# Performance work log

Hardware: AMD Instinct MI355X
Metric: run time of the kernel (lower is better)

Reference implementation:

```python
import jax, jax.numpy as jnp
import numpy as np


def setup_inputs() -> dict:
    key = jax.random.key(0)
    k1, k2, k3, k4, k5 = jax.random.split(key, 5)
    B, C, H, W = 8, 256, 64, 64
    Cp = C // 8  # query/key channels
    x = jax.random.normal(k1, (B, C, H, W), dtype=jnp.float32)
    # 1x1 conv weights (bias=False in the module), spectral norm treated as a fixed weight scale
    Wq = jax.random.normal(k2, (Cp, C), dtype=jnp.float32) * 0.05
    Wk = jax.random.normal(k3, (Cp, C), dtype=jnp.float32) * 0.05
    Wv = jax.random.normal(k4, (C, C), dtype=jnp.float32) * 0.05
    gamma = jax.random.normal(k5, (1,), dtype=jnp.float32)
    return {"x": x, "Wq": Wq, "Wk": Wk, "Wv": Wv, "gamma": gamma}


def reference(x, Wq, Wk, Wv, gamma):
    B, C, H, W = x.shape
    xf = x.reshape(B, C, H * W)  # (B, C, N)
    # ConvLayer = 1x1 conv (no bias) followed by ReLU
    f = jax.nn.relu(jnp.einsum('oc,bcn->bon', Wq, xf))  # (B, C', N)
    g = jax.nn.relu(jnp.einsum('oc,bcn->bon', Wk, xf))  # (B, C', N)
    h = jax.nn.relu(jnp.einsum('oc,bcn->bon', Wv, xf))  # (B, C, N)
    # beta = softmax(f^T g, dim=1): normalize over the FIRST N axis (faithful to source)
    scores = jnp.einsum('bcn,bcm->bnm', f, g)  # (B, N, N)
    beta = jax.nn.softmax(scores, axis=1)
    o = gamma * jnp.einsum('bcn,bnm->bcm', h, beta) + xf  # (B, C, N)
    return o.reshape(B, C, H, W)
```

## Files before the change

### kernel.cpp

```cpp
#include <hip/hip_runtime.h>


typedef __attribute__((ext_vector_type(8))) short bf16x8;
typedef __attribute__((ext_vector_type(4))) float f32x4;
typedef __attribute__((ext_vector_type(4))) unsigned short us4;

#define LOG2E 1.44269504088896f

static __device__ __forceinline__ unsigned short f2bf(float x) {
    union { float f; unsigned u; } v; v.f = x;
    unsigned r = v.u + 0x7FFFu + ((v.u >> 16) & 1u);
    return (unsigned short)(r >> 16);
}
static __device__ __forceinline__ float bf2f(unsigned short u) {
    union { unsigned u; float f; } v; v.u = ((unsigned)u) << 16;
    return v.f;
}

__global__ __launch_bounds__(256) void wconv_kernel(
    const float* __restrict__ Wq, const float* __restrict__ Wk,
    const float* __restrict__ Wv, unsigned short* __restrict__ wq,
    unsigned short* __restrict__ wk, unsigned short* __restrict__ wv)
{
    const int i = blockIdx.x * 256 + threadIdx.x;
    if (i < 8192)            wq[i] = f2bf(Wq[i] * LOG2E);
    else if (i < 16384)      wk[i - 8192] = f2bf(Wk[i - 8192]);
    else                     wv[i - 16384] = f2bf(Wv[i - 16384]);
}

#define XPITCH 264
#define HSPITCH 72
__global__ __launch_bounds__(256, 2) void producer_kernel(
    const float* __restrict__ x, const unsigned short* __restrict__ wq,
    const unsigned short* __restrict__ wk, const unsigned short* __restrict__ wv,
    unsigned short* __restrict__ f_t, unsigned short* __restrict__ g_t,
    unsigned short* __restrict__ h_bf, float* __restrict__ normg,
    float* __restrict__ pmax)
{
    __shared__ unsigned short xh_s[64 * XPITCH];
    __shared__ unsigned short hst[4 * 32 * HSPITCH];
    __shared__ unsigned short fg_s[4 * 2 * 512];

    const int tid  = threadIdx.x;
    const int w    = tid >> 6;
    const int lane = tid & 63;
    const int q    = lane >> 4;
    const int r    = lane & 15;
    const int b    = blockIdx.x & 7;
    const int nt   = blockIdx.x >> 3;
    const int n0   = nt << 6;
    const size_t bN = (size_t)b << 12;
    const f32x4 zero = {0.f, 0.f, 0.f, 0.f};

#pragma unroll
    for (int jj = 0; jj < 4; jj++) {
        const int task = jj * 256 + tid;
        const int n4 = task & 15;
        const int c4 = task >> 4;
        float va[4][4];
#pragma unroll
        for (int i = 0; i < 4; i++) {
            const f32x4 v = __builtin_nontemporal_load(
                (const f32x4*)(x + ((size_t)b << 20)
                               + (size_t)(c4 * 4 + i) * 4096 + n0) + n4);
            va[i][0] = v.x; va[i][1] = v.y; va[i][2] = v.z; va[i][3] = v.w;
        }
#pragma unroll
        for (int i = 0; i < 4; i++) {
            us4 t;
            t.x = f2bf(va[0][i]); t.y = f2bf(va[1][i]);
            t.z = f2bf(va[2][i]); t.w = f2bf(va[3][i]);
            *(us4*)(xh_s + (n4 * 4 + i) * XPITCH + c4 * 4) = t;
        }
    }
    __syncthreads();

    f32x4 accf[2], accg[2];
    accf[0] = accf[1] = accg[0] = accg[1] = zero;

#pragma unroll
    for (int pass = 0; pass < 2; pass++) {
        f32x4 acch[2][4];
#pragma unroll
        for (int cs = 0; cs < 2; cs++)
#pragma unroll
            for (int ns = 0; ns < 4; ns++) acch[cs][ns] = zero;

        for (int ks = 0; ks < 8; ks++) {
            const int kof = ks * 32 + q * 8;
            bf16x8 av0 = *(const bf16x8*)(wv + (size_t)(w * 64 + pass * 32 + r) * 256 + kof);
            bf16x8 av1 = *(const bf16x8*)(wv + (size_t)(w * 64 + pass * 32 + 16 + r) * 256 + kof);
            bf16x8 aq0, aq1, ak0, ak1;
            if (pass == 0) {
                aq0 = *(const bf16x8*)(wq + (size_t)(r) * 256 + kof);
                aq1 = *(const bf16x8*)(wq + (size_t)(16 + r) * 256 + kof);
                ak0 = *(const bf16x8*)(wk + (size_t)(r) * 256 + kof);
                ak1 = *(const bf16x8*)(wk + (size_t)(16 + r) * 256 + kof);
            }
#pragma unroll
            for (int ns = 0; ns < 4; ns++) {
                const bf16x8 bx = *(const bf16x8*)(xh_s + (ns * 16 + r) * XPITCH + kof);
                acch[0][ns] = __builtin_amdgcn_mfma_f32_16x16x32_bf16(av0, bx, acch[0][ns], 0, 0, 0);
                acch[1][ns] = __builtin_amdgcn_mfma_f32_16x16x32_bf16(av1, bx, acch[1][ns], 0, 0, 0);
                if (pass == 0 && ns == w) {
                    accf[0] = __builtin_amdgcn_mfma_f32_16x16x32_bf16(aq0, bx, accf[0], 0, 0, 0);
                    accf[1] = __builtin_amdgcn_mfma_f32_16x16x32_bf16(aq1, bx, accf[1], 0, 0, 0);
                    accg[0] = __builtin_amdgcn_mfma_f32_16x16x32_bf16(ak0, bx, accg[0], 0, 0, 0);
                    accg[1] = __builtin_amdgcn_mfma_f32_16x16x32_bf16(ak1, bx, accg[1], 0, 0, 0);
                }
            }
        }

        if (pass == 0) {
            unsigned short* lf = fg_s + w * 1024;
            unsigned short* lg = lf + 512;
#pragma unroll
            for (int ms = 0; ms < 2; ms++)
#pragma unroll
                for (int reg = 0; reg < 4; reg++) {
                    lf[r * 32 + ms * 16 + q * 4 + reg] = f2bf(fmaxf(accf[ms][reg], 0.f));
                    lg[r * 32 + ms * 16 + q * 4 + reg] = f2bf(fmaxf(accg[ms][reg], 0.f));
                }
            const bf16x8 ffrag = *(const bf16x8*)(lf + r * 32 + q * 8);
            const bf16x8 gfrag = *(const bf16x8*)(lg + r * 32 + q * 8);
            *(bf16x8*)(f_t + ((bN + n0 + w * 16 + r) << 5) + q * 8) = ffrag;
            *(bf16x8*)(g_t + ((bN + n0 + w * 16 + r) << 5) + q * 8) = gfrag;

            float nf2 = 0.f, ng2 = 0.f;
#pragma unroll
            for (int i = 0; i < 8; i++) {
                const float fv = bf2f(((unsigned short*)&ffrag)[i]);
                const float gv = bf2f(((unsigned short*)&gfrag)[i]);
                nf2 += fv * fv; ng2 += gv * gv;
            }
            nf2 += __shfl_xor(nf2, 16); nf2 += __shfl_xor(nf2, 32);
            ng2 += __shfl_xor(ng2, 16); ng2 += __shfl_xor(ng2, 32);
            if (q == 0) normg[bN + n0 + w * 16 + r] = sqrtf(ng2);
            float nf = sqrtf(nf2);
#pragma unroll
            for (int off = 1; off < 16; off <<= 1) nf = fmaxf(nf, __shfl_xor(nf, off));
            if (lane == 0) pmax[(b << 8) + nt * 4 + w] = nf;
        }

        unsigned short* hs = hst + w * (32 * HSPITCH);
#pragma unroll
        for (int cs = 0; cs < 2; cs++)
#pragma unroll
            for (int ns = 0; ns < 4; ns++)
#pragma unroll
                for (int reg = 0; reg < 4; reg++)
                    hs[(cs * 16 + q * 4 + reg) * HSPITCH + ns * 16 + r] =
                        f2bf(fmaxf(acch[cs][ns][reg], 0.f));
        const size_t hdst = (((size_t)(b * 64 + nt)) << 14)
                          + (size_t)(w * 64 + pass * 32) * 64;
#pragma unroll
        for (int p = 0; p < 4; p++) {
            const int cl = p * 8 + (lane >> 3);
            const int kk = lane & 7;
            *(bf16x8*)(h_bf + hdst + cl * 64 + kk * 8) =
                *(const bf16x8*)(hs + cl * HSPITCH + kk * 8);
        }
    }
}

__global__ __launch_bounds__(512, 4) void attn_kernel(
    const unsigned short* __restrict__ f_t, const unsigned short* __restrict__ g_t,
    const unsigned short* __restrict__ h_bf, const float* __restrict__ x,
    const float* __restrict__ gamma, const float* __restrict__ normg,
    const float* __restrict__ pmax, float* __restrict__ out)
{
    __shared__ unsigned short p_s[3][64 * 128];
    __shared__ float red_l[8][64];
    __shared__ float sLi[64];

    const int tid  = threadIdx.x;
    const int w    = tid >> 6;
    const int lane = tid & 63;
    const int q    = lane >> 4;
    const int r    = lane & 15;
    const int b    = blockIdx.x & 7;
    const int m0   = (blockIdx.x >> 3) << 6;

    const size_t bN = (size_t)b << 12;
    const int c0 = w << 5;

    float pv = pmax[(b << 8) + lane];
    pv = fmaxf(pv, pmax[(b << 8) + 64 + lane]);
    pv = fmaxf(pv, pmax[(b << 8) + 128 + lane]);
    pv = fmaxf(pv, pmax[(b << 8) + 192 + lane]);
#pragma unroll
    for (int off = 1; off < 64; off <<= 1) pv = fmaxf(pv, __shfl_xor(pv, off));
    const float mnf = pv;

    bf16x8 bg[4];
    float nMh[4];
#pragma unroll
    for (int ms = 0; ms < 4; ms++) {
        bg[ms] = *(const bf16x8*)(g_t + ((bN + m0 + ms * 16 + r) << 5) + (q << 3));
        nMh[ms] = -(mnf * normg[bN + m0 + ms * 16 + r] * 1.0002f);
    }

    f32x4 acc[2][4];
    const f32x4 zero = {0.f, 0.f, 0.f, 0.f};
#pragma unroll
    for (int cs = 0; cs < 2; cs++)
#pragma unroll
        for (int ms = 0; ms < 4; ms++) acc[cs][ms] = zero;
    float lt[4] = {0.f, 0.f, 0.f, 0.f};

    const int wchunk = (w << 1) + (q >> 1);
    const int wphys  = (wchunk & 8) | ((wchunk ^ r) & 7);
    const int woff   = (wphys << 3) + ((q & 1) << 2);

    auto ldf = [&](int t) {
        return *(const bf16x8*)(f_t + ((bN + (t << 7) + (w << 4) + r) << 5) + (q << 3));
    };
    auto produce = [&](const bf16x8 af, unsigned short* pb) {
#pragma unroll
        for (int ms = 0; ms < 4; ms++) {
            f32x4 ci; ci[0] = ci[1] = ci[2] = ci[3] = nMh[ms];
            const f32x4 sv = __builtin_amdgcn_mfma_f32_16x16x32_bf16(af, bg[ms], ci, 0, 0, 0);
            const float e0 = __builtin_amdgcn_exp2f(sv[0]);
            const float e1 = __builtin_amdgcn_exp2f(sv[1]);
            const float e2 = __builtin_amdgcn_exp2f(sv[2]);
            const float e3 = __builtin_amdgcn_exp2f(sv[3]);
            lt[ms] += (e0 + e1) + (e2 + e3);
            uint2 pk;
            pk.x = __builtin_amdgcn_perm(__float_as_uint(e1), __float_as_uint(e0), 0x07060302u);
            pk.y = __builtin_amdgcn_perm(__float_as_uint(e3), __float_as_uint(e2), 0x07060302u);
            *(uint2*)(pb + ((ms * 16 + r) << 7) + woff) = pk;
        }
    };

    bf16x8 afn = ldf(0);
    produce(afn, p_s[0]);
    afn = ldf(1);

    int sr = 0, sw = 1;
    for (int t = 0; t < 32; t++) {
        __syncthreads();
        bf16x8 ah[2][4];
#pragma unroll
        for (int ch = 0; ch < 4; ch++) {
            const unsigned short* hb =
                h_bf + (((size_t)(b * 64 + t * 2 + (ch >> 1))) << 14) + ((ch & 1) << 5) + (q << 3);
#pragma unroll
            for (int cs = 0; cs < 2; cs++)
                ah[cs][ch] = *(const bf16x8*)(hb + ((c0 + cs * 16 + r) << 6));
        }
        if (t < 31) {
            const bf16x8 afc = afn;
            if (t < 30) afn = ldf(t + 2);
            produce(afc, p_s[sw]);
        }
        const unsigned short* pb = p_s[sr];
#pragma unroll
        for (int ch = 0; ch < 4; ch++) {
            bf16x8 bp[4];
#pragma unroll
            for (int ms = 0; ms < 4; ms++) {
                const int idx  = (ch << 2) + q;
                const int phys = (idx & 8) | ((idx ^ r) & 7);
                bp[ms] = *(const bf16x8*)(pb + ((ms * 16 + r) << 7) + (phys << 3));
            }
            __builtin_amdgcn_s_setprio(1);
#pragma unroll
            for (int cs = 0; cs < 2; cs++)
#pragma unroll
                for (int ms = 0; ms < 4; ms++)
                    acc[cs][ms] = __builtin_amdgcn_mfma_f32_16x16x32_bf16(
                        ah[cs][ch], bp[ms], acc[cs][ms], 0, 0, 0);
            __builtin_amdgcn_s_setprio(0);
        }
        sr = sw;
        sw = (sw == 2) ? 0 : sw + 1;
    }

#pragma unroll
    for (int ms = 0; ms < 4; ms++) {
        lt[ms] += __shfl_xor(lt[ms], 16);
        lt[ms] += __shfl_xor(lt[ms], 32);
    }
    __syncthreads();
    if (q == 0)
#pragma unroll
        for (int ms = 0; ms < 4; ms++) red_l[w][ms * 16 + r] = lt[ms];
    __syncthreads();
    if (tid < 64) {
        float L = 0.f;
#pragma unroll
        for (int ww = 0; ww < 8; ww++) L += red_l[ww][tid];
        sLi[tid] = 1.f / L;
    }
    __syncthreads();

    const float gm = gamma[0];
#pragma unroll
    for (int cs = 0; cs < 2; cs++) {
#pragma unroll
        for (int ms = 0; ms < 4; ms++) {
            const float gl = gm * sLi[ms * 16 + r];
#pragma unroll
            for (int reg = 0; reg < 4; reg++) {
                const int c = c0 + cs * 16 + q * 4 + reg;
                const size_t a = (((size_t)b * 256 + c) << 12) + m0 + ms * 16 + r;
                const float xv = __builtin_nontemporal_load(x + a);
                __builtin_nontemporal_store(gl * acc[cs][ms][reg] + xv, out + a);
            }
        }
    }
}

extern "C" void kernel_launch(void* const* d_in, const int* in_sizes, int n_in,
                              void* d_out, int out_size, void* d_ws, size_t ws_size,
                              hipStream_t stream) {
    const float* x     = (const float*)d_in[0];
    const float* Wq    = (const float*)d_in[1];
    const float* Wk    = (const float*)d_in[2];
    const float* Wv    = (const float*)d_in[3];
    const float* gamma = (const float*)d_in[4];
    float* out = (float*)d_out;

    char* ws = (char*)d_ws;
    unsigned short* f_t  = (unsigned short*)ws;
    unsigned short* g_t  = (unsigned short*)(ws + (2u << 20));
    unsigned short* h_bf = (unsigned short*)(ws + (4u << 20));
    float*          ng   = (float*)(ws + (20u << 20));
    float*          pmx  = (float*)(ws + (20u << 20) + (1u << 17));
    unsigned short* wq   = (unsigned short*)(ws + (21u << 20));
    unsigned short* wk   = wq + 8192;
    unsigned short* wv   = wk + 8192;

    wconv_kernel<<<dim3(320), 256, 0, stream>>>(Wq, Wk, Wv, wq, wk, wv);
    producer_kernel<<<dim3(512), 256, 0, stream>>>(x, wq, wk, wv, f_t, g_t, h_bf, ng, pmx);
    attn_kernel<<<dim3(512), 512, 0, stream>>>(f_t, g_t, h_bf, x, gamma, ng, pmx, out);
}
```

Baseline: 288.0 us.

## Pre-transpose x to bf16 in a prep kernel and read it from global memory

The weight-conversion kernel becomes a prep kernel that also converts x to bf16 and transposes it to an (N, C) layout in workspace using a shared-memory tile. The producer kernel drops its own x staging through LDS and instead loads MFMA B operands straight from the pre-transposed global buffer. The ks loop is fully unrolled, and the setprio hints around the MFMAs in the attention kernel are removed. This frees producer LDS and its sync, which may help occupancy, but adds an extra pass over x plus a 16MB intermediate write and read, and it replaces LDS reads with global reads.

```diff
diff --git a/kernel.cpp b/kernel.cpp
--- a/kernel.cpp
+++ b/kernel.cpp
@@ -17,27 +17,66 @@
     return v.f;
 }
 
-__global__ __launch_bounds__(256) void wconv_kernel(
-    const float* __restrict__ Wq, const float* __restrict__ Wk,
-    const float* __restrict__ Wv, unsigned short* __restrict__ wq,
+__global__ __launch_bounds__(256) void prep_kernel(
+    const float* __restrict__ x, const float* __restrict__ Wq,
+    const float* __restrict__ Wk, const float* __restrict__ Wv,
+    unsigned short* __restrict__ x16t, unsigned short* __restrict__ wq,
     unsigned short* __restrict__ wk, unsigned short* __restrict__ wv)
 {
-    const int i = blockIdx.x * 256 + threadIdx.x;
-    if (i < 8192)            wq[i] = f2bf(Wq[i] * LOG2E);
-    else if (i < 16384)      wk[i - 8192] = f2bf(Wk[i - 8192]);
-    else                     wv[i - 16384] = f2bf(Wv[i - 16384]);
-}
-
-#define XPITCH 264
+    const int bid = blockIdx.x;
+    const int tid = threadIdx.x;
+    if (bid < 2048) {
+        __shared__ unsigned short t_s[64 * 72];
+        const int b  = bid >> 8;
+        const int cb = (bid >> 6) & 3;
+        const int nb = bid & 63;
+        const int c0 = cb << 6, n0 = nb << 6;
+        const int cr = tid >> 4;
+        const int nc = (tid & 15) << 2;
+#pragma unroll
+        for (int i = 0; i < 4; i++) {
+            const int c = cr + i * 16;
+            const f32x4 v = __builtin_nontemporal_load(
+                (const f32x4*)(x + ((size_t)(b * 256 + c0 + c) << 12) + n0 + nc));
+            t_s[(nc + 0) * 72 + c] = f2bf(v.x);
+            t_s[(nc + 1) * 72 + c] = f2bf(v.y);
+            t_s[(nc + 2) * 72 + c] = f2bf(v.z);
+            t_s[(nc + 3) * 72 + c] = f2bf(v.w);
+        }
+        __syncthreads();
+#pragma unroll
+        for (int it = 0; it < 2; it++) {
+            const int k  = it * 256 + tid;
+            const int n  = k >> 3;
+            const int ch = k & 7;
+            const bf16x8 vv = *(const bf16x8*)(t_s + n * 72 + ch * 8);
+            *(bf16x8*)(x16t + (((size_t)(b << 12) + n0 + n) << 8) + c0 + ch * 8) = vv;
+        }
+    } else {
+        const int j = bid - 2048;
+#pragma unroll
+        for (int it = 0; it < 4; it++) {
+            const int e = j * 4096 + it * 1024 + tid * 4;
+            f32x4 v; unsigned short* dst; float sc = 1.f;
+            if (e < 8192)        { v = *(const f32x4*)(Wq + e);          dst = wq + e;          sc = LOG2E; }
+            else if (e < 16384)  { v = *(const f32x4*)(Wk + (e - 8192)); dst = wk + (e - 8192); }
+            else                 { v = *(const f32x4*)(Wv + (e - 16384)); dst = wv + (e - 16384); }
+            us4 o;
+            o.x = f2bf(v.x * sc); o.y = f2bf(v.y * sc);
+            o.z = f2bf(v.z * sc); o.w = f2bf(v.w * sc);
+            *(us4*)dst = o;
+        }
+    }
+}
+
 #define HSPITCH 72
 __global__ __launch_bounds__(256, 2) void producer_kernel(
-    const float* __restrict__ x, const unsigned short* __restrict__ wq,
+    const unsigned short* __restrict__ x16t, const unsigned short* __restrict__ wq,
     const unsigned short* __restrict__ wk, const unsigned short* __restrict__ wv,
     unsigned short* __restrict__ f_t, unsigned short* __restrict__ g_t,
     unsigned short* __restrict__ h_bf, float* __restrict__ normg,
     float* __restrict__ pmax)
 {
-    __shared__ unsigned short xh_s[64 * XPITCH];
     __shared__ unsigned short hst[4 * 32 * HSPITCH];
     __shared__ unsigned short fg_s[4 * 2 * 512];
 
@@ -51,29 +90,7 @@
     const int n0   = nt << 6;
     const size_t bN = (size_t)b << 12;
     const f32x4 zero = {0.f, 0.f, 0.f, 0.f};
-
-#pragma unroll
-    for (int jj = 0; jj < 4; jj++) {
-        const int task = jj * 256 + tid;
-        const int n4 = task & 15;
-        const int c4 = task >> 4;
-        float va[4][4];
-#pragma unroll
-        for (int i = 0; i < 4; i++) {
-            const f32x4 v = __builtin_nontemporal_load(
-                (const f32x4*)(x + ((size_t)b << 20)
-                               + (size_t)(c4 * 4 + i) * 4096 + n0) + n4);
-            va[i][0] = v.x; va[i][1] = v.y; va[i][2] = v.z; va[i][3] = v.w;
-        }
-#pragma unroll
-        for (int i = 0; i < 4; i++) {
-            us4 t;
-            t.x = f2bf(va[0][i]); t.y = f2bf(va[1][i]);
-            t.z = f2bf(va[2][i]); t.w = f2bf(va[3][i]);
-            *(us4*)(xh_s + (n4 * 4 + i) * XPITCH + c4 * 4) = t;
-        }
-    }
-    __syncthreads();
+    const unsigned short* xb = x16t + (((size_t)(b << 12) + n0) << 8);
 
     f32x4 accf[2], accg[2];
     accf[0] = accf[1] = accg[0] = accg[1] = zero;
@@ -86,10 +103,11 @@
 #pragma unroll
             for (int ns = 0; ns < 4; ns++) acch[cs][ns] = zero;
 
+#pragma unroll
         for (int ks = 0; ks < 8; ks++) {
             const int kof = ks * 32 + q * 8;
-            bf16x8 av0 = *(const bf16x8*)(wv + (size_t)(w * 64 + pass * 32 + r) * 256 + kof);
-            bf16x8 av1 = *(const bf16x8*)(wv + (size_t)(w * 64 + pass * 32 + 16 + r) * 256 + kof);
+            const bf16x8 av0 = *(const bf16x8*)(wv + (size_t)(w * 64 + pass * 32 + r) * 256 + kof);
+            const bf16x8 av1 = *(const bf16x8*)(wv + (size_t)(w * 64 + pass * 32 + 16 + r) * 256 + kof);
             bf16x8 aq0, aq1, ak0, ak1;
             if (pass == 0) {
                 aq0 = *(const bf16x8*)(wq + (size_t)(r) * 256 + kof);
@@ -99,7 +117,7 @@
             }
 #pragma unroll
             for (int ns = 0; ns < 4; ns++) {
-                const bf16x8 bx = *(const bf16x8*)(xh_s + (ns * 16 + r) * XPITCH + kof);
+                const bf16x8 bx = *(const bf16x8*)(xb + (size_t)(ns * 16 + r) * 256 + kof);
                 acch[0][ns] = __builtin_amdgcn_mfma_f32_16x16x32_bf16(av0, bx, acch[0][ns], 0, 0, 0);
                 acch[1][ns] = __builtin_amdgcn_mfma_f32_16x16x32_bf16(av1, bx, acch[1][ns], 0, 0, 0);
                 if (pass == 0 && ns == w) {
@@ -263,14 +281,12 @@
                 const int phys = (idx & 8) | ((idx ^ r) & 7);
                 bp[ms] = *(const bf16x8*)(pb + ((ms * 16 + r) << 7) + (phys << 3));
             }
-            __builtin_amdgcn_s_setprio(1);
 #pragma unroll
             for (int cs = 0; cs < 2; cs++)
 #pragma unroll
                 for (int ms = 0; ms < 4; ms++)
                     acc[cs][ms] = __builtin_amdgcn_mfma_f32_16x16x32_bf16(
                         ah[cs][ch], bp[ms], acc[cs][ms], 0, 0, 0);
-            __builtin_amdgcn_s_setprio(0);
         }
         sr = sw;
         sw = (sw == 2) ? 0 : sw + 1;
@@ -330,8 +346,9 @@
     unsigned short* wq   = (unsigned short*)(ws + (21u << 20));
     unsigned short* wk   = wq + 8192;
     unsigned short* wv   = wk + 8192;
-
-    wconv_kernel<<<dim3(320), 256, 0, stream>>>(Wq, Wk, Wv, wq, wk, wv);
-    producer_kernel<<<dim3(512), 256, 0, stream>>>(x, wq, wk, wv, f_t, g_t, h_bf, ng, pmx);
+    unsigned short* x16t = (unsigned short*)(ws + (22u << 20));
+
+    prep_kernel<<<dim3(2068), 256, 0, stream>>>(x, Wq, Wk, Wv, x16t, wq, wk, wv);
+    producer_kernel<<<dim3(512), 256, 0, stream>>>(x16t, wq, wk, wv, f_t, g_t, h_bf, ng, pmx);
     attn_kernel<<<dim3(512), 512, 0, stream>>>(f_t, g_t, h_bf, x, gamma, ng, pmx, out);
 }
```

Result: faster. 264.3 us (-8.2%).
